# Performance work log

Hardware: AMD Instinct MI355X
Metric: run time of the kernel (lower is better)

## Reference

```python
import jax, jax.numpy as jnp
import numpy as np

S, B, C, H, W = 5, 2, 128, 24, 24
N_ITER = 3
BN_EPS = 1e-5


def conv2d(x, w, b, pad):
    # x: (N, Cin, H, W), w: (Cout, Cin, kh, kw)
    y = jax.lax.conv_general_dilated(
        x, w, (1, 1), [(pad, pad), (pad, pad)],
        dimension_numbers=('NCHW', 'OIHW', 'NCHW'))
    return y + b[None, :, None, None]


def setup_inputs() -> dict:
    key = jax.random.key(0)
    ks = jax.random.split(key, 8)
    sc = 0.03  # keep pre-softmax logits in a sane range
    d = {}
    d['x'] = jax.random.normal(ks[0], (S, B, C, H, W), jnp.float32) * 0.5
    d['Wf_w'] = jax.random.normal(ks[1], (C, C, 3, 3), jnp.float32) * sc
    d['Wf_b'] = jnp.zeros((C,), jnp.float32)
    d['Wh_w'] = jax.random.normal(ks[2], (C, C, 3, 3), jnp.float32) * sc
    d['Wh_b'] = jnp.zeros((C,), jnp.float32)
    d['Wl_w'] = jax.random.normal(ks[3], (C, C, 3, 3), jnp.float32) * sc
    d['Wl_b'] = jnp.zeros((C,), jnp.float32)
    d['alpha'] = jnp.ones((1,), jnp.float32)
    d['Wc'] = jax.random.normal(ks[4], (C, C), jnp.float32) * sc
    d['Wg_w'] = jax.random.normal(ks[5], (C, C, 3, 3), jnp.float32) * sc
    d['Wg_b'] = jnp.zeros((C,), jnp.float32)
    d['bn_gamma'] = jnp.ones((C,), jnp.float32)
    d['bn_beta'] = jnp.zeros((C,), jnp.float32)
    d['gru_zr_w'] = jax.random.normal(ks[6], (2 * C, 2 * C, 5, 5), jnp.float32) * sc
    d['gru_zr_b'] = jnp.zeros((2 * C,), jnp.float32)
    d['gru_h_w'] = jax.random.normal(ks[7], (C, 2 * C, 5, 5), jnp.float32) * sc
    d['gru_h_b'] = jnp.zeros((C,), jnp.float32)
    d['intra_w'] = jnp.full((1,), 0.5, jnp.float32)
    d['inter_w'] = jnp.full((1,), 0.5, jnp.float32)
    return d


def reference(x, Wf_w, Wf_b, Wh_w, Wh_b, Wl_w, Wl_b, alpha, Wc, Wg_w, Wg_b,
              bn_gamma, bn_beta, gru_zr_w, gru_zr_b, gru_h_w, gru_h_b,
              intra_w, inter_w):
    S_, B_, C_, H_, W_ = x.shape
    N = H_ * W_
    # BatchNorm2d in inference mode with fresh running stats (mean=0, var=1)
    bn_scale = bn_gamma / jnp.sqrt(1.0 + BN_EPS)
    mask = (1.0 - jnp.eye(S_, dtype=x.dtype))[:, :, None, None, None, None]
    h = x
    for _ in range(N_ITER):
        hb = h.reshape(S_ * B_, C_, H_, W_)
        # ---- intra-node self-attention (per node in sequence) ----
        ft = conv2d(hb, Wf_w, Wf_b, 1).reshape(S_, B_, C_, N)
        ht = conv2d(hb, Wh_w, Wh_b, 1).reshape(S_, B_, C_, N)
        lt = conv2d(hb, Wl_w, Wl_b, 1).reshape(S_, B_, C_, N)
        att = jax.nn.softmax(jnp.einsum('sbcn,sbcm->sbnm', ft, ht), axis=-1)
        ctx = jnp.einsum('sbnm,sbcm->sbcn', att, lt).reshape(S_, B_, C_, H_, W_)
        eii = alpha[0] * ctx + h
        # ---- inter-node pairwise attention messages (all i,j pairs) ----
        hf = h.reshape(S_, B_, C_, N)
        yt = jnp.einsum('cd,jbdn->jbcn', Wc, hf)
        eij = jnp.einsum('ibcn,jbcm->ijbnm', hf, yt)  # (S,S,B,N,N)
        eijn = jax.nn.softmax(eij, axis=-1)
        mji = jnp.einsum('ijbnm,jbcm->ijbcn', eijn, hf)  # (S,S,B,C,N)
        m4 = mji.reshape(S_ * S_ * B_, C_, H_, W_)
        g = jax.nn.sigmoid(jnp.mean(conv2d(m4, Wg_w, Wg_b, 1),
                                    axis=(2, 3), keepdims=True))
        mg = (g * m4) * bn_scale[None, :, None, None] + bn_beta[None, :, None, None]
        mg = mg.reshape(S_, S_, B_, C_, H_, W_)
        inter = jnp.sum(mg * mask, axis=1)  # exclude j == i
        msg = intra_w[0] * eii + inter_w[0] * inter
        # ---- ConvGRU update + residual ----
        xi = msg.reshape(S_ * B_, C_, H_, W_)
        zr = jax.nn.sigmoid(conv2d(jnp.concatenate([xi, hb], axis=1),
                                   gru_zr_w, gru_zr_b, 2))
        z, r = zr[:, :C_], zr[:, C_:]
        h_hat = jnp.tanh(conv2d(jnp.concatenate([xi, r * hb], axis=1),
                                gru_h_w, gru_h_b, 2))
        h_new = (1.0 - z) * hb + z * h_hat
        h = (h_new + hb).reshape(S_, B_, C_, H_, W_)
    return h
```

## Files before the change

### kernel.cpp

```cpp
#include <hip/hip_runtime.h>
#include <math.h>

#define S_  5
#define B_  2
#define C_  128
#define N_  576
#define SB  10
#define NPAIR 40
#define C2  256

typedef short v8s __attribute__((ext_vector_type(8)));
typedef float v4f __attribute__((ext_vector_type(4)));

#define GLOBAL_AS __attribute__((address_space(1)))
#define LDS_AS    __attribute__((address_space(3)))

__device__ __forceinline__ unsigned short f2bf(float f) {
    union { float f; unsigned u; } v; v.f = f;
    unsigned r = (v.u + 0x7FFF + ((v.u >> 16) & 1)) >> 16;
    return (unsigned short)r;
}
__device__ __forceinline__ float bf2f(unsigned short h) {
    union { unsigned u; float f; } v; v.u = ((unsigned)h) << 16;
    return v.f;
}

__device__ __forceinline__ void packA5_body(int idx, const float* __restrict__ w,
                                            unsigned short* __restrict__ Apk, int M)
{
    if (idx >= M * 6400) return;
    int r = idx;
    int j = r & 7;      r >>= 3;
    int quad = r & 3;   r >>= 2;
    int l15 = r & 15;   r >>= 4;
    int c = r & 3;      r >>= 2;
    int tap_l = r % 5;  r /= 5;
    int g = r % 5;      r /= 5;
    int ch = r & 1;     r >>= 1;
    int kk = r & 3;     r >>= 2;
    int cgb = r;
    int co = cgb * 64 + c * 16 + l15;
    int ci = kk * 64 + ch * 32 + quad * 8 + j;
    int tap = g * 5 + tap_l;
    Apk[idx] = f2bf(w[((size_t)co * 256 + ci) * 25 + tap]);
}
__device__ __forceinline__ void packA3_body(int idx, const float* __restrict__ wf,
                                            const float* __restrict__ wh,
                                            const float* __restrict__ wl,
                                            unsigned short* __restrict__ Apk)
{
    if (idx >= 384 * 1152) return;
    int r = idx;
    int j = r & 7;      r >>= 3;
    int quad = r & 3;   r >>= 2;
    int l15 = r & 15;   r >>= 4;
    int c = r & 3;      r >>= 2;
    int tap_l = r % 3;  r /= 3;
    int g = r % 3;      r /= 3;
    int ch = r & 1;     r >>= 1;
    int kk = r & 1;     r >>= 1;
    int cgb = r;
    int co = cgb * 64 + c * 16 + l15;
    const float* w = (co < 128) ? wf : (co < 256) ? wh : wl;
    int cl = co & 127;
    int ci = kk * 64 + ch * 32 + quad * 8 + j;
    int tap = g * 3 + tap_l;
    Apk[idx] = f2bf(w[((size_t)cl * 128 + ci) * 9 + tap]);
}
__device__ __forceinline__ void packWc_body(int idx, const float* __restrict__ w,
                                            unsigned short* __restrict__ o)
{
    if (idx < 128 * 128) o[idx] = f2bf(w[idx]);
}
__device__ __forceinline__ void packWgT_body(int idx, const float* __restrict__ w,
                                             float* __restrict__ o)
{
    if (idx >= 128 * 1152) return;
    int co = idx & 127, i = idx >> 7;
    o[(size_t)i * 128 + co] = w[(size_t)co * 1152 + i];
}

__device__ __forceinline__ void tc_body(
    int px0, int img,
    const float* __restrict__ src, const float* __restrict__ zrp,
    const float* __restrict__ zrb,
    unsigned short* __restrict__ dst, unsigned short* __restrict__ vfd)
{
    const size_t PLANE = (size_t)SB * C2 * N_;
    __shared__ float tile[128][9];
    int t = threadIdx.x;
    #pragma unroll
    for (int i = 0; i < 4; ++i) {
        int e = i * 256 + t; int ci = e >> 3; int px = e & 7;
        float v = src[((size_t)img * 128 + ci) * 576 + px0 + px];
        if (zrp) {
            size_t zi = ((size_t)img * C2 + 128 + ci) * 576 + px0 + px;
            float a = zrb[128 + ci];
            #pragma unroll
            for (int k = 0; k < 4; ++k) a += zrp[k * PLANE + zi];
            v *= 1.f / (1.f + __expf(-a));
        }
        tile[ci][px] = v;
        if (vfd) {
            int m = px0 + px;
            int ctile = ci >> 4, l15v = ci & 15;
            int sIdx = m >> 5, quadv = (m >> 3) & 3, j = m & 7;
            vfd[(((size_t)img * 8 + ctile) * 18 + sIdx) * 512 + (quadv * 16 + l15v) * 8 + j] = f2bf(v);
        }
    }
    __syncthreads();
    #pragma unroll
    for (int i = 0; i < 4; ++i) {
        int e = i * 256 + t; int pxl = e >> 7; int ci = e & 127;
        dst[((size_t)img * 576 + px0 + pxl) * 128 + ci] = f2bf(tile[ci][pxl]);
    }
}

__global__ __launch_bounds__(256) void tc_kernel(
    const float* __restrict__ src, const float* __restrict__ zrp,
    const float* __restrict__ zrb,
    unsigned short* __restrict__ dst, unsigned short* __restrict__ vfd)
{
    tc_body(blockIdx.x * 8, blockIdx.y, src, zrp, zrb, dst, vfd);
}

#define NB_A3   1728
#define NB_A5ZR 6400
#define NB_A5H  3200
#define NB_WC   64
#define NB_WGT  576
#define NB_TC   720
__global__ __launch_bounds__(256) void pack_all_kernel(
    const float* __restrict__ Wf_w, const float* __restrict__ Wh_w,
    const float* __restrict__ Wl_w, unsigned short* __restrict__ Wp3,
    const float* __restrict__ zr_w, unsigned short* __restrict__ Wpzr,
    const float* __restrict__ gh_w, unsigned short* __restrict__ Wph,
    const float* __restrict__ Wc,  unsigned short* __restrict__ Wcb,
    const float* __restrict__ Wg_w, float* __restrict__ WgT,
    const float* __restrict__ x, unsigned short* __restrict__ hT16,
    unsigned short* __restrict__ VFi)
{
    int bid = blockIdx.x, t = threadIdx.x;
    if (bid < NB_A3) {
        packA3_body(bid * 256 + t, Wf_w, Wh_w, Wl_w, Wp3);
    } else if (bid < NB_A3 + NB_A5ZR) {
        packA5_body((bid - NB_A3) * 256 + t, zr_w, Wpzr, 256);
    } else if (bid < NB_A3 + NB_A5ZR + NB_A5H) {
        packA5_body((bid - NB_A3 - NB_A5ZR) * 256 + t, gh_w, Wph, 128);
    } else if (bid < NB_A3 + NB_A5ZR + NB_A5H + NB_WC) {
        packWc_body((bid - NB_A3 - NB_A5ZR - NB_A5H) * 256 + t, Wc, Wcb);
    } else if (bid < NB_A3 + NB_A5ZR + NB_A5H + NB_WC + NB_WGT) {
        packWgT_body((bid - NB_A3 - NB_A5ZR - NB_A5H - NB_WC) * 256 + t, Wg_w, WgT);
    } else {
        int b2 = bid - (NB_A3 + NB_A5ZR + NB_A5H + NB_WC + NB_WGT);
        tc_body((b2 % 72) * 8, b2 / 72, x, nullptr, nullptr, hT16, VFi);
    }
}

template<int KD, int R, int CINT, int SPLITK, int MODE>
__device__ __forceinline__ void conv_body(
    int bx, int by, int bz,
    const unsigned short* __restrict__ srcA, const unsigned short* __restrict__ srcB,
    const unsigned short* __restrict__ Apk, int COUT, float* __restrict__ po,
    const float* __restrict__ b0, const float* __restrict__ b1, const float* __restrict__ b2,
    unsigned short* __restrict__ t0, unsigned short* __restrict__ t1,
    unsigned short* __restrict__ t2)
{
    constexpr int PART   = CINT / SPLITK;
    constexpr int NCH    = PART / 32;
    constexpr int NSUB   = NCH * KD;
    constexpr int WR     = 8 + 2 * R;
    constexpr int WC     = 24 + 2 * R;
    constexpr int NPOS   = WR * WC;
    constexpr int NSLOTB = NPOS * 4;
    constexpr int RB     = (NSLOTB + 255) / 256;
    constexpr int AUNITS = KD * 4 * 64;
    constexpr int AR     = AUNITS / 256;
    __shared__ __align__(16) unsigned short Ab[2][AUNITS * 8];
    __shared__ __align__(16) unsigned short Bb[NPOS * 32];

    int f   = bx;
    int kk  = f % SPLITK;
    int cgb = f / SPLITK;
    int pxb = by;
    int img = bz;
    int t = threadIdx.x;
    int wave = t >> 6, lane = t & 63;
    int quad = lane >> 4, l15 = lane & 15;
    int r0 = pxb * 8;

    const int cibase = kk * PART;
    const unsigned short* src = (cibase >= 128) ? srcB : srcA;
    const int cioff0 = cibase & 127;
    const unsigned short* srcI = src + (size_t)img * 576 * 128;

    int posBase[3], pxs[3];
    #pragma unroll
    for (int s = 0; s < 3; ++s) {
        int px = pxb * 192 + wave * 48 + s * 16 + l15;
        pxs[s] = px;
        int pr = px / 24, pc = px % 24;
        posBase[s] = (pr - r0 + R) * WC + pc + R;
    }

    int goffB[RB]; bool gokB[RB];
    #pragma unroll
    for (int rr = 0; rr < RB; ++rr) {
        int idx = rr * 256 + wave * 64 + lane;
        int pos = idx >> 2, slotq = idx & 3;
        int gr = slotq ^ ((pos >> 1) & 3);
        int wr = pos / WC, wc = pos % WC;
        int grow = r0 - R + wr, gcol = wc - R;
        gokB[rr] = (idx < NSLOTB) && grow >= 0 && grow < 24 && gcol >= 0 && gcol < 24;
        goffB[rr] = (grow * 24 + gcol) * 128 + gr * 8;
    }

    auto stageB = [&](int ch) {
        const unsigned short* sp = srcI + cioff0 + ch * 32;
        #pragma unroll
        for (int rr = 0; rr < RB; ++rr) {
            if (gokB[rr]) {
                __builtin_amdgcn_global_load_lds(
                    (const GLOBAL_AS void*)(sp + goffB[rr]),
                    (LDS_AS void*)((char*)&Bb[0] + (size_t)(rr * 256 + wave * 64) * 16),
                    16, 0, 0);
            }
        }
    };
    auto stageA = [&](int sub, int buf) {
        const unsigned short* sp = Apk + ((size_t)((cgb * SPLITK + kk) * NSUB + sub)) * (AUNITS * 8);
        #pragma unroll
        for (int r = 0; r < AR; ++r) {
            int u0 = r * 256 + wave * 64;
            __builtin_amdgcn_global_load_lds(
                (const GLOBAL_AS void*)(sp + (size_t)(u0 + lane) * 8),
                (LDS_AS void*)((char*)&Ab[buf][0] + (size_t)u0 * 16),
                16, 0, 0);
        }
    };

    v4f acc[4][3];
    #pragma unroll
    for (int c = 0; c < 4; ++c)
        #pragma unroll
        for (int s = 0; s < 3; ++s)
            #pragma unroll
            for (int r = 0; r < 4; ++r) acc[c][s][r] = 0.f;

    {
        v8s zv;
        #pragma unroll
        for (int j = 0; j < 8; ++j) zv[j] = 0;
        for (int i = t; i < NPOS * 4; i += 256) ((v8s*)Bb)[i] = zv;
    }
    __syncthreads();
    stageB(0);
    stageA(0, 0);
    __syncthreads();

    int sub = 0;
    #pragma unroll 1
    for (int ch = 0; ch < NCH; ++ch) {
        #pragma unroll 1
        for (int g = 0; g < KD; ++g) {
            if (sub + 1 < NSUB) stageA(sub + 1, (sub + 1) & 1);
            const unsigned short* Ap = &Ab[sub & 1][0];
            #pragma unroll
            for (int tl = 0; tl < KD; ++tl) {
                int doff = (g - R) * WC + (tl - R);
                v8s a[4];
                #pragma unroll
                for (int c = 0; c < 4; ++c)
                    a[c] = *(const v8s*)&Ap[((tl * 4 + c) * 64 + l15 * 4 + quad) * 8];
                v8s b[3];
                #pragma unroll
                for (int s = 0; s < 3; ++s) {
                    int pos = posBase[s] + doff;
                    b[s] = *(const v8s*)&Bb[pos * 32 + ((quad ^ ((pos >> 1) & 3)) << 3)];
                }
                #pragma unroll
                for (int c = 0; c < 4; ++c)
                    #pragma unroll
                    for (int s = 0; s < 3; ++s)
                        acc[c][s] = __builtin_amdgcn_mfma_f32_16x16x32_bf16(a[c], b[s], acc[c][s], 0, 0, 0);
            }
            __syncthreads();
            ++sub;
        }
        if (ch + 1 < NCH) { stageB(ch + 1); __syncthreads(); }
    }

    if (MODE == 0) {
        float* out = po + (size_t)kk * ((size_t)SB * COUT * 576)
                   + ((size_t)img * COUT + cgb * 64) * 576;
        #pragma unroll
        for (int c = 0; c < 4; ++c)
            #pragma unroll
            for (int s = 0; s < 3; ++s)
                #pragma unroll
                for (int r = 0; r < 4; ++r) {
                    int col = c * 16 + quad * 4 + r;
                    out[(size_t)col * 576 + pxs[s]] = acc[c][s][r];
                }
    } else {
        #pragma unroll
        for (int c = 0; c < 4; ++c)
            #pragma unroll
            for (int s = 0; s < 3; ++s) {
                int px = pxs[s];
                #pragma unroll
                for (int r = 0; r < 4; ++r) {
                    int co = cgb * 64 + c * 16 + quad * 4 + r;
                    int which = co >> 7, cl = co & 127;
                    const float* bp = (which == 0) ? b0 : (which == 1) ? b1 : b2;
                    float v = acc[c][s][r] + bp[cl];
                    if (which == 0) {
                        t0[((size_t)img * 576 + px) * 128 + cl] = f2bf(v);
                    } else if (which == 1) {
                        int mt = px >> 4, l15m = px & 15;
                        int kb = cl >> 5, quadk = (cl >> 3) & 3, jj = cl & 7;
                        t1[(((size_t)img * 36 + mt) * 4 + kb) * 512 + (quadk * 16 + l15m) * 8 + jj] = f2bf(v);
                    } else {
                        int ctile = cl >> 4, l15v = cl & 15;
                        int sIdx = px >> 5, quadv = (px >> 3) & 3, jj = px & 7;
                        t2[(((size_t)img * 8 + ctile) * 18 + sIdx) * 512 + (quadv * 16 + l15v) * 8 + jj] = f2bf(v);
                    }
                }
            }
    }
}

template<int KD, int R, int CINT, int SPLITK, int MODE>
__global__ __launch_bounds__(256, 1) void conv_mfma(
    const unsigned short* __restrict__ srcA, const unsigned short* __restrict__ srcB,
    const unsigned short* __restrict__ Apk, int COUT, float* __restrict__ po,
    const float* __restrict__ b0, const float* __restrict__ b1, const float* __restrict__ b2,
    unsigned short* __restrict__ t0, unsigned short* __restrict__ t1,
    unsigned short* __restrict__ t2)
{
    conv_body<KD, R, CINT, SPLITK, MODE>(blockIdx.x, blockIdx.y, blockIdx.z,
        srcA, srcB, Apk, COUT, po, b0, b1, b2, t0, t1, t2);
}

__device__ __forceinline__ void yt_body(
    int mt, int img,
    const unsigned short* __restrict__ hT, const unsigned short* __restrict__ Wcb,
    unsigned short* __restrict__ KFi)
{
    int t = threadIdx.x, wave = t >> 6, lane = t & 63;
    int q = lane >> 4, l15 = lane & 15;
    int n0 = mt * 16;
    v4f acc[2];
    #pragma unroll
    for (int ct = 0; ct < 2; ++ct)
        #pragma unroll
        for (int r = 0; r < 4; ++r) acc[ct][r] = 0.f;
    #pragma unroll
    for (int kk = 0; kk < 4; ++kk) {
        v8s b = *(const v8s*)(hT + ((size_t)img * 576 + n0 + l15) * 128 + kk * 32 + q * 8);
        #pragma unroll
        for (int ct = 0; ct < 2; ++ct) {
            v8s a = *(const v8s*)(Wcb + (size_t)((wave * 2 + ct) * 16 + l15) * 128 + kk * 32 + q * 8);
            acc[ct] = __builtin_amdgcn_mfma_f32_16x16x32_bf16(a, b, acc[ct], 0, 0, 0);
        }
    }
    #pragma unroll
    for (int ct = 0; ct < 2; ++ct) {
        #pragma unroll
        for (int r = 0; r < 4; ++r) {
            int co = (wave * 2 + ct) * 16 + q * 4 + r;
            int kk = co >> 5, quadk = (co >> 3) & 3, j = co & 7;
            KFi[(((size_t)img * 36 + mt) * 4 + kk) * 512 + (quadk * 16 + l15) * 8 + j]
                = f2bf(acc[ct][r]);
        }
    }
}

__global__ __launch_bounds__(256, 1) void conv3_yt_kernel(
    const unsigned short* __restrict__ hT, const unsigned short* __restrict__ Wp3,
    const float* __restrict__ Wf_b, const float* __restrict__ Wh_b,
    const float* __restrict__ Wl_b,
    unsigned short* __restrict__ ftT, unsigned short* __restrict__ KFa,
    unsigned short* __restrict__ VFa,
    const unsigned short* __restrict__ Wcb, unsigned short* __restrict__ KFi)
{
    int bid = blockIdx.x;
    if (bid < 180) {
        conv_body<3, 1, 128, 1, 1>(bid % 6, (bid / 6) % 3, bid / 18,
            hT, hT, Wp3, 384, nullptr, Wf_b, Wh_b, Wl_b, ftT, KFa, VFa);
    } else {
        int b2 = bid - 180;
        yt_body(b2 % 36, b2 / 36, hT, Wcb, KFi);
    }
}

__global__ __launch_bounds__(256) void attn_merged(
    const unsigned short* __restrict__ QTi, const unsigned short* __restrict__ KFa,
    const unsigned short* __restrict__ VFa, float* __restrict__ Of,
    const float* __restrict__ addsrc, const float* __restrict__ alpha,
    const unsigned short* __restrict__ QTe, const unsigned short* __restrict__ KFe,
    const unsigned short* __restrict__ VFe, unsigned short* __restrict__ Oh,
    float* __restrict__ wpart)
{
    __shared__ __align__(16) unsigned short P[16 * 576];
    __shared__ float redmx[4][16];
    __shared__ float redsm[4][16];
    int t = threadIdx.x;
    int wave = t >> 6, lane = t & 63;
    int q = lane >> 4, l15 = lane & 15;
    int mt = blockIdx.x;
    int n0 = mt * 16;
    int p = blockIdx.y;
    bool intra = (p < SB);
    int pp = 0;
    const unsigned short *Qp, *Kp, *Vp;
    if (intra) {
        Qp = QTi + ((size_t)p * 576 + n0) * 128;
        Kp = KFa + (size_t)p * 36 * 4 * 512;
        Vp = VFa + (size_t)p * 8 * 18 * 512;
    } else {
        pp = p - SB;
        int b = pp & 1; int ij = pp >> 1; int i = ij >> 2; int jj = ij & 3;
        int j = jj + (jj >= i ? 1 : 0);
        int qimg = i * 2 + b, kimg = j * 2 + b;
        Qp = QTe + ((size_t)qimg * 576 + n0) * 128;
        Kp = KFe + (size_t)kimg * 36 * 4 * 512;
        Vp = VFe + (size_t)kimg * 8 * 18 * 512;
    }

    v8s aq[4];
    #pragma unroll
    for (int kk = 0; kk < 4; ++kk)
        aq[kk] = *(const v8s*)(Qp + (size_t)l15 * 128 + kk * 32 + q * 8);

    v4f S[9];
    #pragma unroll
    for (int i = 0; i < 9; ++i)
        #pragma unroll
        for (int r = 0; r < 4; ++r) S[i][r] = 0.f;

    #pragma unroll
    for (int i = 0; i < 9; ++i) {
        int mtk = wave * 9 + i;
        #pragma unroll
        for (int kk = 0; kk < 4; ++kk) {
            v8s b = *(const v8s*)(Kp + ((size_t)(mtk * 4 + kk)) * 512 + lane * 8);
            S[i] = __builtin_amdgcn_mfma_f32_16x16x32_bf16(aq[kk], b, S[i], 0, 0, 0);
        }
    }

    float mx[4];
    #pragma unroll
    for (int r = 0; r < 4; ++r) {
        float m = S[0][r];
        #pragma unroll
        for (int i = 1; i < 9; ++i) m = fmaxf(m, S[i][r]);
        #pragma unroll
        for (int off = 1; off < 16; off <<= 1) m = fmaxf(m, __shfl_xor(m, off));
        mx[r] = m;
    }
    if (l15 == 0) {
        #pragma unroll
        for (int r = 0; r < 4; ++r) redmx[wave][q * 4 + r] = mx[r];
    }
    __syncthreads();
    float sum[4];
    #pragma unroll
    for (int r = 0; r < 4; ++r) {
        float g = fmaxf(fmaxf(redmx[0][q * 4 + r], redmx[1][q * 4 + r]),
                        fmaxf(redmx[2][q * 4 + r], redmx[3][q * 4 + r]));
        float s = 0.f;
        #pragma unroll
        for (int i = 0; i < 9; ++i) { float e = __expf(S[i][r] - g); S[i][r] = e; s += e; }
        #pragma unroll
        for (int off = 1; off < 16; off <<= 1) s += __shfl_xor(s, off);
        sum[r] = s;
    }
    if (l15 == 0) {
        #pragma unroll
        for (int r = 0; r < 4; ++r) redsm[wave][q * 4 + r] = sum[r];
    }
    #pragma unroll
    for (int i = 0; i < 9; ++i) {
        int m = (wave * 9 + i) * 16 + l15;
        int cm = m >> 3, mo = m & 7;
        #pragma unroll
        for (int r = 0; r < 4; ++r) {
            int n = q * 4 + r;
            P[n * 576 + ((cm ^ (n & 7)) << 3) + mo] = f2bf(S[i][r]);
        }
    }
    __syncthreads();
    float inv[4];
    #pragma unroll
    for (int r = 0; r < 4; ++r)
        inv[r] = 1.f / (redsm[0][q * 4 + r] + redsm[1][q * 4 + r] +
                        redsm[2][q * 4 + r] + redsm[3][q * 4 + r]);

    v4f o[2];
    #pragma unroll
    for (int ct = 0; ct < 2; ++ct)
        #pragma unroll
        for (int r = 0; r < 4; ++r) o[ct][r] = 0.f;

    for (int s = 0; s < 18; ++s) {
        int cm = s * 4 + q;
        v8s a = *(const v8s*)&P[l15 * 576 + ((cm ^ (l15 & 7)) << 3)];
        #pragma unroll
        for (int ct = 0; ct < 2; ++ct) {
            int ctile = wave * 2 + ct;
            v8s b = *(const v8s*)(Vp + ((size_t)(ctile * 18 + s)) * 512 + lane * 8);
            o[ct] = __builtin_amdgcn_mfma_f32_16x16x32_bf16(a, b, o[ct], 0, 0, 0);
        }
    }

    if (intra) {
        float al = alpha[0];
        #pragma unroll
        for (int ct = 0; ct < 2; ++ct) {
            int c = (wave * 2 + ct) * 16 + l15;
            size_t base = ((size_t)p * 128 + c) * 576 + n0 + q * 4;
            #pragma unroll
            for (int r = 0; r < 4; ++r)
                Of[base + r] = al * o[ct][r] * inv[r] + addsrc[base + r];
        }
    } else {
        #pragma unroll
        for (int ct = 0; ct < 2; ++ct) {
            int c = (wave * 2 + ct) * 16 + l15;
            size_t base = ((size_t)pp * 128 + c) * 576 + n0 + q * 4;
            float vr[4];
            #pragma unroll
            for (int r = 0; r < 4; ++r) {
                unsigned short hb = f2bf(o[ct][r] * inv[r]);
                Oh[base + r] = hb;
                vr[r] = bf2f(hb);
            }
            float sums[9];
            #pragma unroll
            for (int k = 0; k < 9; ++k) sums[k] = 0.f;
            #pragma unroll
            for (int r = 0; r < 4; ++r) {
                int px = n0 + q * 4 + r;
                int row = px / 24, col = px % 24;
                float v = vr[r];
                sums[0] += v;
                if (row == 0)  sums[1] += v;
                if (row == 23) sums[2] += v;
                if (col == 0)  sums[3] += v;
                if (col == 23) sums[4] += v;
                if (px == 0)   sums[5] += v;
                if (px == 23)  sums[6] += v;
                if (px == 552) sums[7] += v;
                if (px == 575) sums[8] += v;
            }
            #pragma unroll
            for (int k = 0; k < 9; ++k) {
                sums[k] += __shfl_xor(sums[k], 16);
                sums[k] += __shfl_xor(sums[k], 32);
            }
            if (q == 0) {
                float* wp = wpart + (((size_t)pp * 36 + mt) * 9) * 128 + c;
                #pragma unroll
                for (int k = 0; k < 9; ++k) wp[k * 128] = sums[k];
            }
        }
    }
}

__global__ __launch_bounds__(128) void g_kernel(
    const float* __restrict__ wpart, const float* __restrict__ WgT,
    const float* __restrict__ Wgb, float* __restrict__ g)
{
    __shared__ float sw[C_ * 9];
    int pair = blockIdx.x; int co = threadIdx.x;
    float raw[9];
    #pragma unroll
    for (int k = 0; k < 9; ++k) raw[k] = 0.f;
    const float* base = wpart + (size_t)pair * 36 * 9 * 128 + co;
    for (int mt = 0; mt < 36; ++mt) {
        #pragma unroll
        for (int k = 0; k < 9; ++k) raw[k] += base[(mt * 9 + k) * 128];
    }
    float rowsub[3] = {raw[2], 0.f, raw[1]};
    float colsub[3] = {raw[4], 0.f, raw[3]};
    float corner[9] = {raw[8], 0.f, raw[7], 0.f, 0.f, 0.f, raw[6], 0.f, raw[5]};
    #pragma unroll
    for (int ky = 0; ky < 3; ++ky)
        #pragma unroll
        for (int kx = 0; kx < 3; ++kx)
            sw[co * 9 + ky * 3 + kx] = raw[0] - rowsub[ky] - colsub[kx] + corner[ky * 3 + kx];
    __syncthreads();
    float acc = 0.f;
    for (int i = 0; i < C_ * 9; ++i) acc += WgT[(size_t)i * 128 + co] * sw[i];
    float m = acc * (1.f / 576.f) + Wgb[co];
    g[pair * C_ + co] = 1.f / (1.f + __expf(-m));
}

__global__ __launch_bounds__(256) void msg_tc_kernel(
    const float* __restrict__ eii, const unsigned short* __restrict__ mji,
    const float* __restrict__ g, const float* __restrict__ bn_gamma,
    const float* __restrict__ bn_beta, const float* __restrict__ intra_w,
    const float* __restrict__ inter_w, unsigned short* __restrict__ msgT)
{
    __shared__ float tile[128][9];
    int img = blockIdx.y, px0 = blockIdx.x * 8, t = threadIdx.x;
    int s = img >> 1, b = img & 1;
    float iw = intra_w[0], ew = inter_w[0];
    #pragma unroll
    for (int i = 0; i < 4; ++i) {
        int e = i * 256 + t; int ci = e >> 3; int pxl = e & 7;
        int px = px0 + pxl;
        float scale = bn_gamma[ci] * rsqrtf(1.f + 1e-5f);
        float acc = 0.f;
        #pragma unroll
        for (int jj = 0; jj < 4; ++jj) {
            int pidx = (s * 4 + jj) * 2 + b;
            acc += g[pidx * C_ + ci] * bf2f(mji[((size_t)pidx * C_ + ci) * N_ + px]);
        }
        float inter = scale * acc + 4.f * bn_beta[ci];
        tile[ci][pxl] = iw * eii[((size_t)img * C_ + ci) * N_ + px] + ew * inter;
    }
    __syncthreads();
    #pragma unroll
    for (int i = 0; i < 4; ++i) {
        int e = i * 256 + t; int pxl = e >> 7; int ci = e & 127;
        msgT[((size_t)img * 576 + px0 + pxl) * 128 + ci] = f2bf(tile[ci][pxl]);
    }
}

__global__ __launch_bounds__(256) void update_tc_kernel(
    const float* __restrict__ zrp, const float* __restrict__ zrb,
    const float* __restrict__ hhp, const float* __restrict__ ghb,
    const float* __restrict__ h, float* __restrict__ out,
    unsigned short* __restrict__ hTn, unsigned short* __restrict__ VFn, int last)
{
    const size_t ZP = (size_t)SB * C2 * N_;
    const size_t HP = (size_t)SB * C_ * N_;
    __shared__ float tile[128][9];
    int img = blockIdx.y, px0 = blockIdx.x * 8, t = threadIdx.x;
    #pragma unroll
    for (int i = 0; i < 4; ++i) {
        int e = i * 256 + t; int ci = e >> 3; int pxl = e & 7;
        int px = px0 + pxl;
        size_t zi = ((size_t)img * C2 + ci) * N_ + px;
        float za = zrb[ci];
        #pragma unroll
        for (int k = 0; k < 4; ++k) za += zrp[k * ZP + zi];
        float z = 1.f / (1.f + __expf(-za));
        size_t hi = ((size_t)img * C_ + ci) * N_ + px;
        float ha = ghb[ci];
        #pragma unroll
        for (int k = 0; k < 4; ++k) ha += hhp[k * HP + hi];
        float hh = tanhf(ha);
        float o = (2.f - z) * h[hi] + z * hh;
        out[hi] = o;
        tile[ci][pxl] = o;
        if (!last) {
            int ctile = ci >> 4, l15v = ci & 15;
            int sIdx = px >> 5, quadv = (px >> 3) & 3, j = px & 7;
            VFn[(((size_t)img * 8 + ctile) * 18 + sIdx) * 512 + (quadv * 16 + l15v) * 8 + j] = f2bf(o);
        }
    }
    if (!last) {
        __syncthreads();
        #pragma unroll
        for (int i = 0; i < 4; ++i) {
            int e = i * 256 + t; int pxl = e >> 7; int ci = e & 127;
            hTn[((size_t)img * 576 + px0 + pxl) * 128 + ci] = f2bf(tile[ci][pxl]);
        }
    }
}

extern "C" void kernel_launch(void* const* d_in, const int* in_sizes, int n_in,
                              void* d_out, int out_size, void* d_ws, size_t ws_size,
                              hipStream_t stream)
{
    const float* x      = (const float*)d_in[0];
    const float* Wf_w   = (const float*)d_in[1];
    const float* Wf_b   = (const float*)d_in[2];
    const float* Wh_w   = (const float*)d_in[3];
    const float* Wh_b   = (const float*)d_in[4];
    const float* Wl_w   = (const float*)d_in[5];
    const float* Wl_b   = (const float*)d_in[6];
    const float* alpha  = (const float*)d_in[7];
    const float* Wc     = (const float*)d_in[8];
    const float* Wg_w   = (const float*)d_in[9];
    const float* Wg_b   = (const float*)d_in[10];
    const float* bng    = (const float*)d_in[11];
    const float* bnb    = (const float*)d_in[12];
    const float* zr_w   = (const float*)d_in[13];
    const float* zr_b   = (const float*)d_in[14];
    const float* gh_w   = (const float*)d_in[15];
    const float* gh_b   = (const float*)d_in[16];
    const float* intraw = (const float*)d_in[17];
    const float* interw = (const float*)d_in[18];
    float* outp = (float*)d_out;

    float* f = (float*)d_ws;
    const size_t SZ = (size_t)SB * C_ * N_;
    float* hbuf  = f; f += SZ;
    float* eii   = f; f += SZ;
    float* zrp   = f; f += 4 * (size_t)SB * C2 * N_;
    float* hhp   = f; f += 4 * SZ;
    float* wpart = f; f += (size_t)NPAIR * 36 * 9 * 128;
    float* gbuf  = f; f += (size_t)NPAIR * C_;
    float* WgT   = f; f += (size_t)128 * 1152;
    unsigned short* us = (unsigned short*)f;
    unsigned short* mji16  = us; us += (size_t)NPAIR * C_ * N_;
    unsigned short* hT16   = us; us += SZ;
    unsigned short* hc16   = us; us += SZ;
    unsigned short* msgT16 = us; us += SZ;
    unsigned short* ftT    = us; us += SZ;
    unsigned short* KFa    = us; us += SZ;
    unsigned short* VFa    = us; us += SZ;
    unsigned short* Wp3    = us; us += (size_t)384 * 1152;
    unsigned short* Wpzr   = us; us += (size_t)256 * 6400;
    unsigned short* Wph    = us; us += (size_t)128 * 6400;
    unsigned short* Wcb    = us; us += (size_t)128 * 128;
    unsigned short* KFi    = us; us += SZ;

    unsigned short* VFi    = hc16;
    unsigned short* rhbT16 = hc16;

    pack_all_kernel<<<NB_A3 + NB_A5ZR + NB_A5H + NB_WC + NB_WGT + NB_TC, 256, 0, stream>>>(
        Wf_w, Wh_w, Wl_w, Wp3, zr_w, Wpzr, gh_w, Wph, Wc, Wcb, Wg_w, WgT,
        x, hT16, VFi);

    const float* hcur = x;
    for (int it = 0; it < 3; ++it) {
        float* hout = (it == 2) ? outp : hbuf;

        conv3_yt_kernel<<<540, 256, 0, stream>>>(
            hT16, Wp3, Wf_b, Wh_b, Wl_b, ftT, KFa, VFa, Wcb, KFi);
        attn_merged<<<dim3(36, SB + NPAIR), 256, 0, stream>>>(
            ftT, KFa, VFa, eii, hcur, alpha, hT16, KFi, VFi, mji16, wpart);
        g_kernel<<<NPAIR, 128, 0, stream>>>(wpart, WgT, Wg_b, gbuf);
        msg_tc_kernel<<<dim3(72, SB), 256, 0, stream>>>(
            eii, mji16, gbuf, bng, bnb, intraw, interw, msgT16);
        conv_mfma<5, 2, 256, 4, 0><<<dim3(16, 3, SB), 256, 0, stream>>>(
            msgT16, hT16, Wpzr, 256, zrp, nullptr, nullptr, nullptr, nullptr, nullptr, nullptr);
        tc_kernel<<<dim3(72, SB), 256, 0, stream>>>(hcur, zrp, zr_b, rhbT16, nullptr);
        conv_mfma<5, 2, 256, 4, 0><<<dim3(8, 3, SB), 256, 0, stream>>>(
            msgT16, rhbT16, Wph, 128, hhp, nullptr, nullptr, nullptr, nullptr, nullptr, nullptr);
        update_tc_kernel<<<dim3(72, SB), 256, 0, stream>>>(
            zrp, zr_b, hhp, gh_b, hcur, hout, hT16, VFi, (it == 2) ? 1 : 0);
        hcur = hout;
    }
}
```

Baseline: 568.4 us.

## Read conv weights directly from global, double-buffer input tile, split g_kernel reduction

The 5x5 conv kernel stops staging weight sub-tiles through LDS and loads the A fragments straight from the pre-packed global buffer. The freed LDS double-buffers the input tile, so the next channel chunk is prefetched during compute, leaving one barrier per chunk instead of one per kernel row. Launch bounds on the conv kernels now ask for two blocks per CU. g_kernel uses 256 threads, splitting both its partial-sum reduction and its dot product in half and combining them through shared memory. The trade is more global and L2 weight traffic and register pressure in exchange for fewer barriers and more overlap.

```diff
diff --git a/kernel.cpp b/kernel.cpp
--- a/kernel.cpp
+++ b/kernel.cpp
@@ -175,9 +175,7 @@
     constexpr int NSLOTB = NPOS * 4;
     constexpr int RB     = (NSLOTB + 255) / 256;
     constexpr int AUNITS = KD * 4 * 64;
-    constexpr int AR     = AUNITS / 256;
-    __shared__ __align__(16) unsigned short Ab[2][AUNITS * 8];
-    __shared__ __align__(16) unsigned short Bb[NPOS * 32];
+    __shared__ __align__(16) unsigned short Bb[2][NPOS * 32];
 
     int f   = bx;
     int kk  = f % SPLITK;
@@ -215,29 +213,18 @@
         goffB[rr] = (grow * 24 + gcol) * 128 + gr * 8;
     }
 
-    auto stageB = [&](int ch) {
+    auto stageB = [&](int ch, int buf) {
         const unsigned short* sp = srcI + cioff0 + ch * 32;
         #pragma unroll
         for (int rr = 0; rr < RB; ++rr) {
             if (gokB[rr]) {
                 __builtin_amdgcn_global_load_lds(
                     (const GLOBAL_AS void*)(sp + goffB[rr]),
-                    (LDS_AS void*)((char*)&Bb[0] + (size_t)(rr * 256 + wave * 64) * 16),
+                    (LDS_AS void*)((char*)&Bb[buf][0] + (size_t)(rr * 256 + wave * 64) * 16),
                     16, 0, 0);
             }
         }
     };
-    auto stageA = [&](int sub, int buf) {
-        const unsigned short* sp = Apk + ((size_t)((cgb * SPLITK + kk) * NSUB + sub)) * (AUNITS * 8);
-        #pragma unroll
-        for (int r = 0; r < AR; ++r) {
-            int u0 = r * 256 + wave * 64;
-            __builtin_amdgcn_global_load_lds(
-                (const GLOBAL_AS void*)(sp + (size_t)(u0 + lane) * 8),
-                (LDS_AS void*)((char*)&Ab[buf][0] + (size_t)u0 * 16),
-                16, 0, 0);
-        }
-    };
 
     v4f acc[4][3];
     #pragma unroll
@@ -251,32 +238,36 @@
         v8s zv;
         #pragma unroll
         for (int j = 0; j < 8; ++j) zv[j] = 0;
-        for (int i = t; i < NPOS * 4; i += 256) ((v8s*)Bb)[i] = zv;
-    }
-    __syncthreads();
-    stageB(0);
-    stageA(0, 0);
-    __syncthreads();
-
-    int sub = 0;
+        for (int i = t; i < NPOS * 8; i += 256) ((v8s*)Bb)[i] = zv;
+    }
+    __syncthreads();
+    stageB(0, 0);
+    __syncthreads();
+
+    const unsigned short* Abase = Apk
+        + (size_t)(cgb * SPLITK + kk) * NSUB * (AUNITS * 8)
+        + (size_t)(l15 * 4 + quad) * 8;
+
     #pragma unroll 1
     for (int ch = 0; ch < NCH; ++ch) {
+        if (ch + 1 < NCH) stageB(ch + 1, (ch + 1) & 1);
+        const unsigned short* Bcur = &Bb[ch & 1][0];
+        const unsigned short* Ach = Abase + (size_t)(ch * KD) * (AUNITS * 8);
         #pragma unroll 1
         for (int g = 0; g < KD; ++g) {
-            if (sub + 1 < NSUB) stageA(sub + 1, (sub + 1) & 1);
-            const unsigned short* Ap = &Ab[sub & 1][0];
+            const unsigned short* Ag = Ach + (size_t)g * (AUNITS * 8);
             #pragma unroll
             for (int tl = 0; tl < KD; ++tl) {
                 int doff = (g - R) * WC + (tl - R);
                 v8s a[4];
                 #pragma unroll
                 for (int c = 0; c < 4; ++c)
-                    a[c] = *(const v8s*)&Ap[((tl * 4 + c) * 64 + l15 * 4 + quad) * 8];
+                    a[c] = *(const v8s*)(Ag + (size_t)(tl * 4 + c) * 512);
                 v8s b[3];
                 #pragma unroll
                 for (int s = 0; s < 3; ++s) {
                     int pos = posBase[s] + doff;
-                    b[s] = *(const v8s*)&Bb[pos * 32 + ((quad ^ ((pos >> 1) & 3)) << 3)];
+                    b[s] = *(const v8s*)&Bcur[pos * 32 + ((quad ^ ((pos >> 1) & 3)) << 3)];
                 }
                 #pragma unroll
                 for (int c = 0; c < 4; ++c)
@@ -284,10 +275,8 @@
                     for (int s = 0; s < 3; ++s)
                         acc[c][s] = __builtin_amdgcn_mfma_f32_16x16x32_bf16(a[c], b[s], acc[c][s], 0, 0, 0);
             }
-            __syncthreads();
-            ++sub;
-        }
-        if (ch + 1 < NCH) { stageB(ch + 1); __syncthreads(); }
+        }
+        if (ch + 1 < NCH) __syncthreads();
     }
 
     if (MODE == 0) {
@@ -331,7 +320,7 @@
 }
 
 template<int KD, int R, int CINT, int SPLITK, int MODE>
-__global__ __launch_bounds__(256, 1) void conv_mfma(
+__global__ __launch_bounds__(256, 2) void conv_mfma(
     const unsigned short* __restrict__ srcA, const unsigned short* __restrict__ srcB,
     const unsigned short* __restrict__ Apk, int COUT, float* __restrict__ po,
     const float* __restrict__ b0, const float* __restrict__ b1, const float* __restrict__ b2,
@@ -376,7 +365,7 @@
     }
 }
 
-__global__ __launch_bounds__(256, 1) void conv3_yt_kernel(
+__global__ __launch_bounds__(256, 2) void conv3_yt_kernel(
     const unsigned short* __restrict__ hT, const unsigned short* __restrict__ Wp3,
     const float* __restrict__ Wf_b, const float* __restrict__ Wh_b,
     const float* __restrict__ Wl_b,
@@ -568,33 +557,50 @@
     }
 }
 
-__global__ __launch_bounds__(128) void g_kernel(
+__global__ __launch_bounds__(256) void g_kernel(
     const float* __restrict__ wpart, const float* __restrict__ WgT,
     const float* __restrict__ Wgb, float* __restrict__ g)
 {
     __shared__ float sw[C_ * 9];
-    int pair = blockIdx.x; int co = threadIdx.x;
+    __shared__ float acc2[256];
+    int pair = blockIdx.x; int t = threadIdx.x;
+    int co = t & 127, half = t >> 7;
+    const float* base = wpart + (size_t)pair * 36 * 9 * 128 + co;
     float raw[9];
     #pragma unroll
     for (int k = 0; k < 9; ++k) raw[k] = 0.f;
-    const float* base = wpart + (size_t)pair * 36 * 9 * 128 + co;
-    for (int mt = 0; mt < 36; ++mt) {
+    for (int mt = half; mt < 36; mt += 2) {
         #pragma unroll
         for (int k = 0; k < 9; ++k) raw[k] += base[(mt * 9 + k) * 128];
     }
-    float rowsub[3] = {raw[2], 0.f, raw[1]};
-    float colsub[3] = {raw[4], 0.f, raw[3]};
-    float corner[9] = {raw[8], 0.f, raw[7], 0.f, 0.f, 0.f, raw[6], 0.f, raw[5]};
-    #pragma unroll
-    for (int ky = 0; ky < 3; ++ky)
-        #pragma unroll
-        for (int kx = 0; kx < 3; ++kx)
-            sw[co * 9 + ky * 3 + kx] = raw[0] - rowsub[ky] - colsub[kx] + corner[ky * 3 + kx];
+    if (half == 1) {
+        #pragma unroll
+        for (int k = 0; k < 9; ++k) sw[co * 9 + k] = raw[k];
+    }
+    __syncthreads();
+    if (half == 0) {
+        #pragma unroll
+        for (int k = 0; k < 9; ++k) raw[k] += sw[co * 9 + k];
+        float rowsub[3] = {raw[2], 0.f, raw[1]};
+        float colsub[3] = {raw[4], 0.f, raw[3]};
+        float corner[9] = {raw[8], 0.f, raw[7], 0.f, 0.f, 0.f, raw[6], 0.f, raw[5]};
+        #pragma unroll
+        for (int ky = 0; ky < 3; ++ky)
+            #pragma unroll
+            for (int kx = 0; kx < 3; ++kx)
+                sw[co * 9 + ky * 3 + kx] = raw[0] - rowsub[ky] - colsub[kx] + corner[ky * 3 + kx];
+    }
     __syncthreads();
     float acc = 0.f;
-    for (int i = 0; i < C_ * 9; ++i) acc += WgT[(size_t)i * 128 + co] * sw[i];
-    float m = acc * (1.f / 576.f) + Wgb[co];
-    g[pair * C_ + co] = 1.f / (1.f + __expf(-m));
+    const float* wg = WgT + (size_t)half * 576 * 128 + co;
+    const float* swh = sw + half * 576;
+    for (int i = 0; i < 576; ++i) acc += wg[(size_t)i * 128] * swh[i];
+    acc2[t] = acc;
+    __syncthreads();
+    if (half == 0) {
+        float m = (acc + acc2[t + 128]) * (1.f / 576.f) + Wgb[co];
+        g[pair * C_ + co] = 1.f / (1.f + __expf(-m));
+    }
 }
 
 __global__ __launch_bounds__(256) void msg_tc_kernel(
@@ -735,7 +741,7 @@
             hT16, Wp3, Wf_b, Wh_b, Wl_b, ftT, KFa, VFa, Wcb, KFi);
         attn_merged<<<dim3(36, SB + NPAIR), 256, 0, stream>>>(
             ftT, KFa, VFa, eii, hcur, alpha, hT16, KFi, VFi, mji16, wpart);
-        g_kernel<<<NPAIR, 128, 0, stream>>>(wpart, WgT, Wg_b, gbuf);
+        g_kernel<<<NPAIR, 256, 0, stream>>>(wpart, WgT, Wg_b, gbuf);
         msg_tc_kernel<<<dim3(72, SB), 256, 0, stream>>>(
             eii, mji16, gbuf, bng, bnb, intraw, interw, msgT16);
         conv_mfma<5, 2, 256, 4, 0><<<dim3(16, 3, SB), 256, 0, stream>>>(
```

After: 586.7 us. +3.2%, slower.

## Process two query tiles per attention block and split g_kernel reduction across halves

Applied to the files above, without the earlier changes.

The attention kernel now handles 32 query rows per block (two 16-row MFMA tiles) instead of 16. Each K and V fragment loaded from global memory feeds two MFMAs, halving K/V traffic per query and halving the grid to 18x50 blocks. The partial-sum buffer shrinks accordingly. g_kernel now uses 256 threads, with two halves splitting both the partial reduction and the 1152-long weight dot product, to cut its serial latency. The risks are higher register and LDS use (P doubles to about 36KB), which may lower occupancy, and fewer blocks (900) to fill the GPU.

```diff
diff --git a/kernel.cpp b/kernel.cpp
--- a/kernel.cpp
+++ b/kernel.cpp
@@ -402,14 +402,14 @@
     const unsigned short* __restrict__ VFe, unsigned short* __restrict__ Oh,
     float* __restrict__ wpart)
 {
-    __shared__ __align__(16) unsigned short P[16 * 576];
-    __shared__ float redmx[4][16];
-    __shared__ float redsm[4][16];
+    __shared__ __align__(16) unsigned short P[32 * 576];
+    __shared__ float redmx[4][32];
+    __shared__ float redsm[4][32];
     int t = threadIdx.x;
     int wave = t >> 6, lane = t & 63;
     int q = lane >> 4, l15 = lane & 15;
-    int mt = blockIdx.x;
-    int n0 = mt * 16;
+    int mt2 = blockIdx.x;
+    int n0 = mt2 * 32;
     int p = blockIdx.y;
     bool intra = (p < SB);
     int pp = 0;
@@ -428,16 +428,20 @@
         Vp = VFe + (size_t)kimg * 8 * 18 * 512;
     }
 
-    v8s aq[4];
-    #pragma unroll
-    for (int kk = 0; kk < 4; ++kk)
-        aq[kk] = *(const v8s*)(Qp + (size_t)l15 * 128 + kk * 32 + q * 8);
-
-    v4f S[9];
-    #pragma unroll
-    for (int i = 0; i < 9; ++i)
-        #pragma unroll
-        for (int r = 0; r < 4; ++r) S[i][r] = 0.f;
+    v8s aq[2][4];
+    #pragma unroll
+    for (int qt = 0; qt < 2; ++qt)
+        #pragma unroll
+        for (int kk = 0; kk < 4; ++kk)
+            aq[qt][kk] = *(const v8s*)(Qp + (size_t)(qt * 16 + l15) * 128 + kk * 32 + q * 8);
+
+    v4f S[2][9];
+    #pragma unroll
+    for (int qt = 0; qt < 2; ++qt)
+        #pragma unroll
+        for (int i = 0; i < 9; ++i)
+            #pragma unroll
+            for (int r = 0; r < 4; ++r) S[qt][i][r] = 0.f;
 
     #pragma unroll
     for (int i = 0; i < 9; ++i) {
@@ -445,114 +449,129 @@
         #pragma unroll
         for (int kk = 0; kk < 4; ++kk) {
             v8s b = *(const v8s*)(Kp + ((size_t)(mtk * 4 + kk)) * 512 + lane * 8);
-            S[i] = __builtin_amdgcn_mfma_f32_16x16x32_bf16(aq[kk], b, S[i], 0, 0, 0);
-        }
-    }
-
-    float mx[4];
-    #pragma unroll
-    for (int r = 0; r < 4; ++r) {
-        float m = S[0][r];
-        #pragma unroll
-        for (int i = 1; i < 9; ++i) m = fmaxf(m, S[i][r]);
-        #pragma unroll
-        for (int off = 1; off < 16; off <<= 1) m = fmaxf(m, __shfl_xor(m, off));
-        mx[r] = m;
+            S[0][i] = __builtin_amdgcn_mfma_f32_16x16x32_bf16(aq[0][kk], b, S[0][i], 0, 0, 0);
+            S[1][i] = __builtin_amdgcn_mfma_f32_16x16x32_bf16(aq[1][kk], b, S[1][i], 0, 0, 0);
+        }
+    }
+
+    #pragma unroll
+    for (int qt = 0; qt < 2; ++qt) {
+        #pragma unroll
+        for (int r = 0; r < 4; ++r) {
+            float m = S[qt][0][r];
+            #pragma unroll
+            for (int i = 1; i < 9; ++i) m = fmaxf(m, S[qt][i][r]);
+            #pragma unroll
+            for (int off = 1; off < 16; off <<= 1) m = fmaxf(m, __shfl_xor(m, off));
+            if (l15 == 0) redmx[wave][qt * 16 + q * 4 + r] = m;
+        }
+    }
+    __syncthreads();
+    float sum[2][4];
+    #pragma unroll
+    for (int qt = 0; qt < 2; ++qt) {
+        #pragma unroll
+        for (int r = 0; r < 4; ++r) {
+            int rr = qt * 16 + q * 4 + r;
+            float g = fmaxf(fmaxf(redmx[0][rr], redmx[1][rr]),
+                            fmaxf(redmx[2][rr], redmx[3][rr]));
+            float s = 0.f;
+            #pragma unroll
+            for (int i = 0; i < 9; ++i) { float e = __expf(S[qt][i][r] - g); S[qt][i][r] = e; s += e; }
+            #pragma unroll
+            for (int off = 1; off < 16; off <<= 1) s += __shfl_xor(s, off);
+            sum[qt][r] = s;
+        }
     }
     if (l15 == 0) {
         #pragma unroll
-        for (int r = 0; r < 4; ++r) redmx[wave][q * 4 + r] = mx[r];
-    }
-    __syncthreads();
-    float sum[4];
-    #pragma unroll
-    for (int r = 0; r < 4; ++r) {
-        float g = fmaxf(fmaxf(redmx[0][q * 4 + r], redmx[1][q * 4 + r]),
-                        fmaxf(redmx[2][q * 4 + r], redmx[3][q * 4 + r]));
-        float s = 0.f;
-        #pragma unroll
-        for (int i = 0; i < 9; ++i) { float e = __expf(S[i][r] - g); S[i][r] = e; s += e; }
-        #pragma unroll
-        for (int off = 1; off < 16; off <<= 1) s += __shfl_xor(s, off);
-        sum[r] = s;
-    }
-    if (l15 == 0) {
-        #pragma unroll
-        for (int r = 0; r < 4; ++r) redsm[wave][q * 4 + r] = sum[r];
-    }
-    #pragma unroll
-    for (int i = 0; i < 9; ++i) {
-        int m = (wave * 9 + i) * 16 + l15;
-        int cm = m >> 3, mo = m & 7;
+        for (int qt = 0; qt < 2; ++qt)
+            #pragma unroll
+            for (int r = 0; r < 4; ++r) redsm[wave][qt * 16 + q * 4 + r] = sum[qt][r];
+    }
+    #pragma unroll
+    for (int qt = 0; qt < 2; ++qt) {
+        #pragma unroll
+        for (int i = 0; i < 9; ++i) {
+            int m = (wave * 9 + i) * 16 + l15;
+            int cm = m >> 3, mo = m & 7;
+            #pragma unroll
+            for (int r = 0; r < 4; ++r) {
+                int n = qt * 16 + q * 4 + r;
+                P[n * 576 + ((cm ^ (n & 7)) << 3) + mo] = f2bf(S[qt][i][r]);
+            }
+        }
+    }
+    __syncthreads();
+    float inv[2][4];
+    #pragma unroll
+    for (int qt = 0; qt < 2; ++qt)
         #pragma unroll
         for (int r = 0; r < 4; ++r) {
-            int n = q * 4 + r;
-            P[n * 576 + ((cm ^ (n & 7)) << 3) + mo] = f2bf(S[i][r]);
-        }
-    }
-    __syncthreads();
-    float inv[4];
-    #pragma unroll
-    for (int r = 0; r < 4; ++r)
-        inv[r] = 1.f / (redsm[0][q * 4 + r] + redsm[1][q * 4 + r] +
-                        redsm[2][q * 4 + r] + redsm[3][q * 4 + r]);
-
-    v4f o[2];
-    #pragma unroll
-    for (int ct = 0; ct < 2; ++ct)
-        #pragma unroll
-        for (int r = 0; r < 4; ++r) o[ct][r] = 0.f;
+            int rr = qt * 16 + q * 4 + r;
+            inv[qt][r] = 1.f / (redsm[0][rr] + redsm[1][rr] + redsm[2][rr] + redsm[3][rr]);
+        }
+
+    v4f o[2][2];
+    #pragma unroll
+    for (int qt = 0; qt < 2; ++qt)
+        #pragma unroll
+        for (int ct = 0; ct < 2; ++ct)
+            #pragma unroll
+            for (int r = 0; r < 4; ++r) o[qt][ct][r] = 0.f;
 
     for (int s = 0; s < 18; ++s) {
         int cm = s * 4 + q;
-        v8s a = *(const v8s*)&P[l15 * 576 + ((cm ^ (l15 & 7)) << 3)];
+        v8s a0 = *(const v8s*)&P[l15 * 576 + ((cm ^ (l15 & 7)) << 3)];
+        v8s a1 = *(const v8s*)&P[(16 + l15) * 576 + ((cm ^ (l15 & 7)) << 3)];
         #pragma unroll
         for (int ct = 0; ct < 2; ++ct) {
             int ctile = wave * 2 + ct;
             v8s b = *(const v8s*)(Vp + ((size_t)(ctile * 18 + s)) * 512 + lane * 8);
-            o[ct] = __builtin_amdgcn_mfma_f32_16x16x32_bf16(a, b, o[ct], 0, 0, 0);
+            o[0][ct] = __builtin_amdgcn_mfma_f32_16x16x32_bf16(a0, b, o[0][ct], 0, 0, 0);
+            o[1][ct] = __builtin_amdgcn_mfma_f32_16x16x32_bf16(a1, b, o[1][ct], 0, 0, 0);
         }
     }
 
     if (intra) {
         float al = alpha[0];
         #pragma unroll
+        for (int qt = 0; qt < 2; ++qt)
+            #pragma unroll
+            for (int ct = 0; ct < 2; ++ct) {
+                int c = (wave * 2 + ct) * 16 + l15;
+                size_t base = ((size_t)p * 128 + c) * 576 + n0 + qt * 16 + q * 4;
+                #pragma unroll
+                for (int r = 0; r < 4; ++r)
+                    Of[base + r] = al * o[qt][ct][r] * inv[qt][r] + addsrc[base + r];
+            }
+    } else {
+        #pragma unroll
         for (int ct = 0; ct < 2; ++ct) {
             int c = (wave * 2 + ct) * 16 + l15;
-            size_t base = ((size_t)p * 128 + c) * 576 + n0 + q * 4;
-            #pragma unroll
-            for (int r = 0; r < 4; ++r)
-                Of[base + r] = al * o[ct][r] * inv[r] + addsrc[base + r];
-        }
-    } else {
-        #pragma unroll
-        for (int ct = 0; ct < 2; ++ct) {
-            int c = (wave * 2 + ct) * 16 + l15;
-            size_t base = ((size_t)pp * 128 + c) * 576 + n0 + q * 4;
-            float vr[4];
-            #pragma unroll
-            for (int r = 0; r < 4; ++r) {
-                unsigned short hb = f2bf(o[ct][r] * inv[r]);
-                Oh[base + r] = hb;
-                vr[r] = bf2f(hb);
-            }
             float sums[9];
             #pragma unroll
             for (int k = 0; k < 9; ++k) sums[k] = 0.f;
             #pragma unroll
-            for (int r = 0; r < 4; ++r) {
-                int px = n0 + q * 4 + r;
-                int row = px / 24, col = px % 24;
-                float v = vr[r];
-                sums[0] += v;
-                if (row == 0)  sums[1] += v;
-                if (row == 23) sums[2] += v;
-                if (col == 0)  sums[3] += v;
-                if (col == 23) sums[4] += v;
-                if (px == 0)   sums[5] += v;
-                if (px == 23)  sums[6] += v;
-                if (px == 552) sums[7] += v;
-                if (px == 575) sums[8] += v;
+            for (int qt = 0; qt < 2; ++qt) {
+                size_t base = ((size_t)pp * 128 + c) * 576 + n0 + qt * 16 + q * 4;
+                #pragma unroll
+                for (int r = 0; r < 4; ++r) {
+                    unsigned short hb = f2bf(o[qt][ct][r] * inv[qt][r]);
+                    Oh[base + r] = hb;
+                    float v = bf2f(hb);
+                    int px = n0 + qt * 16 + q * 4 + r;
+                    int row = px / 24, col = px % 24;
+                    sums[0] += v;
+                    if (row == 0)  sums[1] += v;
+                    if (row == 23) sums[2] += v;
+                    if (col == 0)  sums[3] += v;
+                    if (col == 23) sums[4] += v;
+                    if (px == 0)   sums[5] += v;
+                    if (px == 23)  sums[6] += v;
+                    if (px == 552) sums[7] += v;
+                    if (px == 575) sums[8] += v;
+                }
             }
             #pragma unroll
             for (int k = 0; k < 9; ++k) {
@@ -560,7 +579,7 @@
                 sums[k] += __shfl_xor(sums[k], 32);
             }
             if (q == 0) {
-                float* wp = wpart + (((size_t)pp * 36 + mt) * 9) * 128 + c;
+                float* wp = wpart + (((size_t)pp * 18 + mt2) * 9) * 128 + c;
                 #pragma unroll
                 for (int k = 0; k < 9; ++k) wp[k * 128] = sums[k];
             }
@@ -568,33 +587,50 @@
     }
 }
 
-__global__ __launch_bounds__(128) void g_kernel(
+__global__ __launch_bounds__(256) void g_kernel(
     const float* __restrict__ wpart, const float* __restrict__ WgT,
     const float* __restrict__ Wgb, float* __restrict__ g)
 {
     __shared__ float sw[C_ * 9];
-    int pair = blockIdx.x; int co = threadIdx.x;
+    __shared__ float acc2[256];
+    int pair = blockIdx.x; int t = threadIdx.x;
+    int co = t & 127, half = t >> 7;
+    const float* base = wpart + (size_t)pair * 18 * 9 * 128 + co;
     float raw[9];
     #pragma unroll
     for (int k = 0; k < 9; ++k) raw[k] = 0.f;
-    const float* base = wpart + (size_t)pair * 36 * 9 * 128 + co;
-    for (int mt = 0; mt < 36; ++mt) {
+    for (int mt = half; mt < 18; mt += 2) {
         #pragma unroll
         for (int k = 0; k < 9; ++k) raw[k] += base[(mt * 9 + k) * 128];
     }
-    float rowsub[3] = {raw[2], 0.f, raw[1]};
-    float colsub[3] = {raw[4], 0.f, raw[3]};
-    float corner[9] = {raw[8], 0.f, raw[7], 0.f, 0.f, 0.f, raw[6], 0.f, raw[5]};
-    #pragma unroll
-    for (int ky = 0; ky < 3; ++ky)
-        #pragma unroll
-        for (int kx = 0; kx < 3; ++kx)
-            sw[co * 9 + ky * 3 + kx] = raw[0] - rowsub[ky] - colsub[kx] + corner[ky * 3 + kx];
+    if (half == 1) {
+        #pragma unroll
+        for (int k = 0; k < 9; ++k) sw[co * 9 + k] = raw[k];
+    }
+    __syncthreads();
+    if (half == 0) {
+        #pragma unroll
+        for (int k = 0; k < 9; ++k) raw[k] += sw[co * 9 + k];
+        float rowsub[3] = {raw[2], 0.f, raw[1]};
+        float colsub[3] = {raw[4], 0.f, raw[3]};
+        float corner[9] = {raw[8], 0.f, raw[7], 0.f, 0.f, 0.f, raw[6], 0.f, raw[5]};
+        #pragma unroll
+        for (int ky = 0; ky < 3; ++ky)
+            #pragma unroll
+            for (int kx = 0; kx < 3; ++kx)
+                sw[co * 9 + ky * 3 + kx] = raw[0] - rowsub[ky] - colsub[kx] + corner[ky * 3 + kx];
+    }
     __syncthreads();
     float acc = 0.f;
-    for (int i = 0; i < C_ * 9; ++i) acc += WgT[(size_t)i * 128 + co] * sw[i];
-    float m = acc * (1.f / 576.f) + Wgb[co];
-    g[pair * C_ + co] = 1.f / (1.f + __expf(-m));
+    const float* wg = WgT + (size_t)half * 576 * 128 + co;
+    const float* swh = sw + half * 576;
+    for (int i = 0; i < 576; ++i) acc += wg[(size_t)i * 128] * swh[i];
+    acc2[t] = acc;
+    __syncthreads();
+    if (half == 0) {
+        float m = (acc + acc2[t + 128]) * (1.f / 576.f) + Wgb[co];
+        g[pair * C_ + co] = 1.f / (1.f + __expf(-m));
+    }
 }
 
 __global__ __launch_bounds__(256) void msg_tc_kernel(
@@ -703,7 +739,7 @@
     float* eii   = f; f += SZ;
     float* zrp   = f; f += 4 * (size_t)SB * C2 * N_;
     float* hhp   = f; f += 4 * SZ;
-    float* wpart = f; f += (size_t)NPAIR * 36 * 9 * 128;
+    float* wpart = f; f += (size_t)NPAIR * 18 * 9 * 128;
     float* gbuf  = f; f += (size_t)NPAIR * C_;
     float* WgT   = f; f += (size_t)128 * 1152;
     unsigned short* us = (unsigned short*)f;
@@ -733,9 +769,9 @@
 
         conv3_yt_kernel<<<540, 256, 0, stream>>>(
             hT16, Wp3, Wf_b, Wh_b, Wl_b, ftT, KFa, VFa, Wcb, KFi);
-        attn_merged<<<dim3(36, SB + NPAIR), 256, 0, stream>>>(
+        attn_merged<<<dim3(18, SB + NPAIR), 256, 0, stream>>>(
             ftT, KFa, VFa, eii, hcur, alpha, hT16, KFi, VFi, mji16, wpart);
-        g_kernel<<<NPAIR, 128, 0, stream>>>(wpart, WgT, Wg_b, gbuf);
+        g_kernel<<<NPAIR, 256, 0, stream>>>(wpart, WgT, Wg_b, gbuf);
         msg_tc_kernel<<<dim3(72, SB), 256, 0, stream>>>(
             eii, mji16, gbuf, bng, bnb, intraw, interw, msgT16);
         conv_mfma<5, 2, 256, 4, 0><<<dim3(16, 3, SB), 256, 0, stream>>>(
```

Result: faster. 525.2 us (-7.6%).
